# Performance work log

Hardware: AMD Instinct MI355X
Metric: run time of the kernel (lower is better)

## Reference

```python
import jax, jax.numpy as jnp
import numpy as np

N_GRAPHS = 256
EPS = 1e-5


def _bn(x, g, b):
    # training-mode BatchNorm1d: biased batch statistics
    m = jnp.mean(x, axis=0)
    v = jnp.mean((x - m) ** 2, axis=0)
    return (x - m) * jax.lax.rsqrt(v + EPS) * g + b


def _gcn_conv(x, W, b, src, dst, dinv, n_nodes):
    # GCNConv: D^{-1/2} (A + I) D^{-1/2} X W + b
    h = x @ W  # [N, H]
    coef = dinv[src] * dinv[dst]  # [E]
    msg = h[src] * coef[:, None]  # [E, H]
    agg = jax.ops.segment_sum(msg, dst, num_segments=n_nodes)
    agg = agg + h * (dinv * dinv)[:, None]  # self-loop term
    return agg + b


def setup_inputs() -> dict:
    key = jax.random.key(0)
    ks = jax.random.split(key, 20)
    N, E, D, H, C = 50000, 600000, 128, 128, 10
    L = 3  # num_conv_layers
    x = jax.random.normal(ks[0], (N, D), dtype=jnp.float32)
    edge_index = jax.random.randint(ks[1], (2, E), 0, N, dtype=jnp.int64)
    batch = jnp.sort(jax.random.randint(ks[2], (N,), 0, N_GRAPHS, dtype=jnp.int64))

    def xavier(k, shape):
        fan_in, fan_out = shape[0], shape[1]
        lim = float(np.sqrt(6.0 / (fan_in + fan_out)))
        return jax.random.uniform(k, shape, jnp.float32, -lim, lim)

    return {
        "x": x,
        "edge_index": edge_index,
        "batch": batch,
        "bn_feat_g": jnp.ones((D,), jnp.float32),
        "bn_feat_b": jnp.full((D,), 1e-4, jnp.float32),
        "conv_feat_W": xavier(ks[3], (D, H)),
        "conv_feat_b": jnp.zeros((H,), jnp.float32),
        "conv_W": jnp.stack([xavier(ks[4 + i], (H, H)) for i in range(L)]),
        "conv_b": jnp.zeros((L, H), jnp.float32),
        "bn_conv_g": jnp.ones((L, H), jnp.float32),
        "bn_conv_b": jnp.full((L, H), 1e-4, jnp.float32),
        "gate_W1": xavier(ks[8], (H, H)),
        "gate_b1": jnp.zeros((H,), jnp.float32),
        "gate_W2": xavier(ks[9], (H, 1)),
        "gate_b2": jnp.zeros((1,), jnp.float32),
        "fc_W": xavier(ks[10], (H, H)),
        "fc_b": jnp.zeros((H,), jnp.float32),
        "bn_fc_g": jnp.ones((H,), jnp.float32),
        "bn_fc_b": jnp.full((H,), 1e-4, jnp.float32),
        "cls_W": xavier(ks[11], (H, C)),
        "cls_b": jnp.zeros((C,), jnp.float32),
    }


def reference(x, edge_index, batch, bn_feat_g, bn_feat_b, conv_feat_W, conv_feat_b,
              conv_W, conv_b, bn_conv_g, bn_conv_b, gate_W1, gate_b1, gate_W2,
              gate_b2, fc_W, fc_b, bn_fc_g, bn_fc_b, cls_W, cls_b):
    N = x.shape[0]
    src, dst = edge_index[0], edge_index[1]
    # degree incl. self-loop (edge weights = 1)
    deg = jax.ops.segment_sum(jnp.ones_like(src, dtype=x.dtype), dst, num_segments=N) + 1.0
    dinv = jax.lax.rsqrt(deg)

    h = _bn(x, bn_feat_g, bn_feat_b)
    h = jax.nn.relu(_gcn_conv(h, conv_feat_W, conv_feat_b, src, dst, dinv, N))
    for i in range(conv_W.shape[0]):
        h = jax.nn.relu(_gcn_conv(_bn(h, bn_conv_g[i], bn_conv_b[i]),
                                  conv_W[i], conv_b[i], src, dst, dinv, N))
    gate = jax.nn.sigmoid(jax.nn.relu(h @ gate_W1 + gate_b1) @ gate_W2 + gate_b2)  # [N,1]
    g = jax.ops.segment_sum(h * gate, batch, num_segments=N_GRAPHS)  # [G, H]
    g = jax.nn.relu(_bn(g, bn_fc_g, bn_fc_b) @ fc_W + fc_b)
    logits = g @ cls_W + cls_b
    return jax.nn.log_softmax(logits, axis=-1)
```

## Files before the change

kernel.cpp:

```cpp
#include <hip/hip_runtime.h>
#include <hip/hip_fp16.h>

typedef unsigned short u16;
typedef unsigned int u32;
typedef __attribute__((ext_vector_type(8))) short short8;
typedef __attribute__((ext_vector_type(4))) float floatx4;

#define EPSI 1e-5f

__device__ __forceinline__ float b2f(u16 h) { return __uint_as_float(((u32)h) << 16); }
__device__ __forceinline__ u16 f2b(float f) {
    u32 u = __float_as_uint(f);
    return (u16)((u + 0x7fffu + ((u >> 16) & 1u)) >> 16);
}
__device__ __forceinline__ u32 pack2(float a, float b) {
    return (u32)f2b(a) | ((u32)f2b(b) << 16);
}
__device__ __forceinline__ float ldf(const void* p, int i, int fm) {
    if (fm == 1) return b2f(((const u16*)p)[i]);
    if (fm == 2) return __half2float(__ushort_as_half(((const u16*)p)[i]));
    return ((const float*)p)[i];
}
__device__ __forceinline__ int ldi(const void* p, int i, int im) {
    return im ? ((const int*)p)[2 * i] : ((const int*)p)[i];
}

__global__ void init_kernel(u32* zp, int nz, const void* ones, const void* ei, int* flags) {
    int i = blockIdx.x * 256 + threadIdx.x;
    if (i < nz) zp[i] = 0;
    if (blockIdx.x == 0 && threadIdx.x == 0) {
        u32 w = ((const u32*)ones)[0];
        int fm = 0;
        if (w == 0x3F803F80u) fm = 1;
        else if (w == 0x3C003C00u) fm = 2;
        const u32* e = (const u32*)ei;
        int all0 = 1;
        for (int k = 0; k < 16; ++k)
            if (e[2 * k + 1] != 0u) all0 = 0;
        flags[0] = fm;
        flags[1] = all0;
    }
}

__global__ void bigprep_kernel(const void* __restrict__ ei, int* __restrict__ cnt, int E,
                               const void* __restrict__ batch, int* __restrict__ bounds, int N,
                               int EB, const void* __restrict__ x, u32* __restrict__ A2,
                               float* __restrict__ stats0, const void* __restrict__ gW1,
                               const void* __restrict__ gb1, u16* __restrict__ Wtg,
                               float* __restrict__ bias2g, const void* __restrict__ cfW,
                               const void* __restrict__ cW, float* __restrict__ WTf,
                               const void* __restrict__ fcW, float* __restrict__ fcWf,
                               const void* __restrict__ clsW, float* __restrict__ clsWf,
                               const void* __restrict__ fcb, float* __restrict__ fcbf,
                               const void* __restrict__ clsb, float* __restrict__ clsbf,
                               const void* __restrict__ gW2, float* __restrict__ gW2f,
                               const void* __restrict__ gb2, float* __restrict__ gb2f,
                               const int* __restrict__ flags) {
    int fm = flags[0];
    int bid = blockIdx.x, t = threadIdx.x;
    if (bid < EB) {
        int im = flags[1];
        int g = bid * 256 + t;
        if (g < E) atomicAdd(&cnt[ldi(ei, E + g, im)], 1);
        if (g < N) {
            int b = ldi(batch, g, im);
            if (g == 0) {
                for (int q = 0; q <= b; ++q) bounds[q] = 0;
            } else {
                int bp = ldi(batch, g - 1, im);
                for (int q = bp + 1; q <= b; ++q) bounds[q] = g;
            }
            if (g == N - 1) {
                for (int q = b + 1; q <= 256; ++q) bounds[q] = N;
            }
        }
        return;
    }
    int pid = bid - EB;
    if (pid < 512) {
        int np = N * 64;
        float s0 = 0.f, s1 = 0.f, q0 = 0.f, q1 = 0.f;
        if (fm == 1) {
            const u32* xs = (const u32*)x;
            for (int j = pid * 256 + t; j < np; j += 512 * 256) {
                u32 w = xs[j];
                A2[j] = w;
                float v0 = b2f((u16)w), v1 = b2f((u16)(w >> 16));
                s0 += v0;
                q0 += v0 * v0;
                s1 += v1;
                q1 += v1 * v1;
            }
        } else {
            for (int j = pid * 256 + t; j < np; j += 512 * 256) {
                float v0 = ldf(x, 2 * j, fm);
                float v1 = ldf(x, 2 * j + 1, fm);
                A2[j] = pack2(v0, v1);
                s0 += v0;
                q0 += v0 * v0;
                s1 += v1;
                q1 += v1 * v1;
            }
        }
        __shared__ float2 sh[256];
        sh[t] = make_float2(s0, s1);
        __syncthreads();
        float* so = stats0 + (pid & 7) * 256;
        if (t < 64) {
            float a = 0.f, b = 0.f;
#pragma unroll
            for (int w = 0; w < 4; ++w) {
                float2 v = sh[t + w * 64];
                a += v.x;
                b += v.y;
            }
            atomicAdd(&so[2 * t], a);
            atomicAdd(&so[2 * t + 1], b);
        }
        __syncthreads();
        sh[t] = make_float2(q0, q1);
        __syncthreads();
        if (t < 64) {
            float a = 0.f, b = 0.f;
#pragma unroll
            for (int w = 0; w < 4; ++w) {
                float2 v = sh[t + w * 64];
                a += v.x;
                b += v.y;
            }
            atomicAdd(&so[128 + 2 * t], a);
            atomicAdd(&so[128 + 2 * t + 1], b);
        }
    } else if (pid < 640) {
        int n = pid - 512;
        if (t < 128) Wtg[n * 128 + t] = f2b(ldf(gW1, t * 128 + n, fm));
        if (t == 0) bias2g[n] = ldf(gb1, n, fm);
    } else if (pid < 704) {
        int task = pid - 640;
        int mat = task >> 4, tile = task & 15;
        int tr = (tile >> 2) * 32, tc = (tile & 3) * 32;
        const void* src = mat == 0 ? cfW : cW;
        int soff = mat == 0 ? 0 : (mat - 1) * 16384;
        __shared__ float tb[32][33];
#pragma unroll
        for (int i = 0; i < 4; ++i) {
            int o = t * 4 + i;
            int r = o >> 5, c = o & 31;
            tb[r][c] = ldf(src, soff + (tr + r) * 128 + tc + c, fm);
        }
        __syncthreads();
        float* dst = WTf + mat * 16384;
#pragma unroll
        for (int i = 0; i < 4; ++i) {
            int o = t * 4 + i;
            int nr = o >> 5, kc = o & 31;
            dst[(tc + nr) * 128 + tr + kc] = tb[kc][nr];
        }
    } else if (pid < 712) {
        int base = (pid - 704) * 2048;
        for (int i = t; i < 2048; i += 256) fcWf[base + i] = ldf(fcW, base + i, fm);
    } else {
        for (int i = t; i < 1280; i += 256) clsWf[i] = ldf(clsW, i, fm);
        if (t < 128) {
            fcbf[t] = ldf(fcb, t, fm);
            gW2f[t] = ldf(gW2, t, fm);
        }
        if (t < 10) clsbf[t] = ldf(clsb, t, fm);
        if (t == 0) gb2f[0] = ldf(gb2, 0, fm);
    }
}

__global__ void scan_part_kernel(const int* __restrict__ cnt, int* __restrict__ part, int n) {
    int b = blockIdx.x, t = threadIdx.x;
    int base = b * 1024 + t * 4;
    int s = 0;
#pragma unroll
    for (int j = 0; j < 4; ++j) {
        int idx = base + j;
        if (idx < n) s += cnt[idx];
    }
    __shared__ int sh[256];
    sh[t] = s;
    __syncthreads();
    for (int o = 128; o > 0; o >>= 1) {
        if (t < o) sh[t] += sh[t + o];
        __syncthreads();
    }
    if (t == 0) part[b] = sh[0];
}

__global__ void scan_local_wprep_kernel(const int* __restrict__ cnt,
                                        const int* __restrict__ part,
                                        int* __restrict__ row_start, int n, int NB,
                                        const float* __restrict__ stats0,
                                        const void* __restrict__ bng,
                                        const void* __restrict__ bnb,
                                        const float* __restrict__ WTf, u16* __restrict__ Wt,
                                        float* __restrict__ bias2, int N,
                                        const int* __restrict__ flags) {
    int b = blockIdx.x, t = threadIdx.x;
    __shared__ int sh[256];
    if (b == NB) {
        int fm = flags[0];
        __shared__ float scl[128], shl[128];
        if (t < 128) {
            float ms = 0.f, qs = 0.f;
#pragma unroll
            for (int c = 0; c < 8; ++c) {
                ms += stats0[c * 256 + t];
                qs += stats0[c * 256 + 128 + t];
            }
            float m = ms / (float)N;
            float var = qs / (float)N - m * m;
            float rs = rsqrtf(var + EPSI);
            float sc = rs * ldf(bng, t, fm);
            scl[t] = sc;
            shl[t] = ldf(bnb, t, fm) - m * sc;
        }
        __syncthreads();
        for (int idx = t; idx < 16384; idx += 256) Wt[idx] = f2b(scl[idx & 127] * WTf[idx]);
        if (t < 128) {
            float acc = 0.f;
#pragma unroll 8
            for (int k = 0; k < 128; ++k) acc += shl[k] * WTf[t * 128 + k];
            bias2[t] = acc;
        }
        return;
    }
    sh[t] = (t < b) ? part[t] : 0;
    __syncthreads();
    for (int o = 128; o > 0; o >>= 1) {
        if (t < o) sh[t] += sh[t + o];
        __syncthreads();
    }
    int pre = sh[0];
    __syncthreads();
    int base = b * 1024 + t * 4;
    int v[4];
    int s = 0;
#pragma unroll
    for (int j = 0; j < 4; ++j) {
        int idx = base + j;
        v[j] = (idx < n) ? cnt[idx] : 0;
        s += v[j];
    }
    sh[t] = s;
    __syncthreads();
    for (int o = 1; o < 256; o <<= 1) {
        int add = (t >= o) ? sh[t - o] : 0;
        __syncthreads();
        sh[t] += add;
        __syncthreads();
    }
    int run = pre + sh[t] - s;
#pragma unroll
    for (int j = 0; j < 4; ++j) {
        int idx = base + j;
        run += v[j];
        if (idx < n) row_start[idx + 1] = run;
    }
    if (b == 0 && t == 0) row_start[0] = 0;
}

__global__ void wprep_kernel(const float* __restrict__ stats, const void* __restrict__ bng,
                             const void* __restrict__ bnb, int poff,
                             const float* __restrict__ WTf, u16* __restrict__ Wt,
                             float* __restrict__ bias2, int N, const int* __restrict__ flags) {
    int fm = flags[0];
    int n = blockIdx.x, k = threadIdx.x;
    float ms = 0.f, qs = 0.f;
#pragma unroll
    for (int c = 0; c < 8; ++c) {
        ms += stats[c * 256 + k];
        qs += stats[c * 256 + 128 + k];
    }
    float m = ms / (float)N;
    float var = qs / (float)N - m * m;
    float rs = rsqrtf(var + EPSI);
    float sc = rs * ldf(bng, poff + k, fm);
    float sh = ldf(bnb, poff + k, fm) - m * sc;
    float w = WTf[n * 128 + k];
    Wt[n * 128 + k] = f2b(sc * w);
    __shared__ float red[128];
    red[k] = sh * w;
    __syncthreads();
    for (int o = 64; o > 0; o >>= 1) {
        if (k < o) red[k] += red[k + o];
        __syncthreads();
    }
    if (k == 0) bias2[n] = red[0];
}

__global__ __launch_bounds__(256) void mfma_fill_kernel(
    const u16* __restrict__ A, const u16* __restrict__ Wt, const float* __restrict__ bias2,
    u16* __restrict__ C, int N, int mmgrid, const void* __restrict__ ei,
    const int* __restrict__ row_start, int* __restrict__ fill_cnt, const int* __restrict__ cnt,
    int* __restrict__ col_idx, float* __restrict__ coef, int E,
    const int* __restrict__ flags) {
    int t = threadIdx.x;
    if ((int)blockIdx.x >= mmgrid) {
        int im = flags[1];
        int e = (blockIdx.x - mmgrid) * 256 + t;
        if (e < E) {
            int s = ldi(ei, e, im);
            int d = ldi(ei, E + e, im);
            int p = row_start[d] + atomicAdd(&fill_cnt[d], 1);
            col_idx[p] = s;
            coef[p] = rsqrtf((float)cnt[s] + 1.0f) * rsqrtf((float)cnt[d] + 1.0f);
        }
        return;
    }
    int wid = t >> 6, lane = t & 63;
    int m16 = lane & 15, q = lane >> 4;
    int row0 = blockIdx.x * 64 + wid * 16;
    if (row0 >= N) return;
    int arow = row0 + m16;
    floatx4 acc[8];
#pragma unroll
    for (int i = 0; i < 8; ++i) acc[i] = (floatx4){0.f, 0.f, 0.f, 0.f};
#pragma unroll
    for (int kc = 0; kc < 4; ++kc) {
        short8 af;
        if (arow < N) {
            af = *(const short8*)&A[(size_t)arow * 128 + kc * 32 + q * 8];
        } else {
#pragma unroll
            for (int j = 0; j < 8; ++j) af[j] = 0;
        }
#pragma unroll
        for (int nt = 0; nt < 8; ++nt) {
            short8 bf = *(const short8*)&Wt[(nt * 16 + m16) * 128 + kc * 32 + q * 8];
            acc[nt] = __builtin_amdgcn_mfma_f32_16x16x32_bf16(af, bf, acc[nt], 0, 0, 0);
        }
    }
#pragma unroll
    for (int nt = 0; nt < 8; ++nt) {
        float b2v = bias2[nt * 16 + m16];
#pragma unroll
        for (int reg = 0; reg < 4; ++reg) {
            int r = row0 + q * 4 + reg;
            if (r < N) C[(size_t)r * 128 + nt * 16 + m16] = f2b(acc[nt][reg] + b2v);
        }
    }
}

__global__ __launch_bounds__(256) void mfma_mm_kernel(
    const u16* __restrict__ A, const u16* __restrict__ Wt, const float* __restrict__ bias2,
    u16* __restrict__ C, float* __restrict__ gate, const float* __restrict__ gW2f,
    const float* __restrict__ gb2f, int N, int mode) {
    int t = threadIdx.x;
    int wid = t >> 6, lane = t & 63;
    int m16 = lane & 15, q = lane >> 4;
    int row0 = blockIdx.x * 64 + wid * 16;
    if (row0 >= N) return;
    int arow = row0 + m16;
    floatx4 acc[8];
#pragma unroll
    for (int i = 0; i < 8; ++i) acc[i] = (floatx4){0.f, 0.f, 0.f, 0.f};
#pragma unroll
    for (int kc = 0; kc < 4; ++kc) {
        short8 af;
        if (arow < N) {
            af = *(const short8*)&A[(size_t)arow * 128 + kc * 32 + q * 8];
        } else {
#pragma unroll
            for (int j = 0; j < 8; ++j) af[j] = 0;
        }
#pragma unroll
        for (int nt = 0; nt < 8; ++nt) {
            short8 bf = *(const short8*)&Wt[(nt * 16 + m16) * 128 + kc * 32 + q * 8];
            acc[nt] = __builtin_amdgcn_mfma_f32_16x16x32_bf16(af, bf, acc[nt], 0, 0, 0);
        }
    }
    if (mode == 0) {
#pragma unroll
        for (int nt = 0; nt < 8; ++nt) {
            float b2v = bias2[nt * 16 + m16];
#pragma unroll
            for (int reg = 0; reg < 4; ++reg) {
                int r = row0 + q * 4 + reg;
                if (r < N) C[(size_t)r * 128 + nt * 16 + m16] = f2b(acc[nt][reg] + b2v);
            }
        }
    } else {
        float p[4] = {0.f, 0.f, 0.f, 0.f};
#pragma unroll
        for (int nt = 0; nt < 8; ++nt) {
            float b2v = bias2[nt * 16 + m16];
            float w2v = gW2f[nt * 16 + m16];
#pragma unroll
            for (int reg = 0; reg < 4; ++reg)
                p[reg] += fmaxf(acc[nt][reg] + b2v, 0.0f) * w2v;
        }
        float gb = gb2f[0];
#pragma unroll
        for (int reg = 0; reg < 4; ++reg) {
            float v = p[reg];
            v += __shfl_xor(v, 1);
            v += __shfl_xor(v, 2);
            v += __shfl_xor(v, 4);
            v += __shfl_xor(v, 8);
            if (m16 == 0) {
                int r = row0 + q * 4 + reg;
                if (r < N) gate[r] = 1.0f / (1.0f + expf(-(v + gb)));
            }
        }
    }
}

__global__ __launch_bounds__(1024) void agg_kernel(
    const u32* __restrict__ C2, const int* __restrict__ row_start,
    const int* __restrict__ col_idx, const float* __restrict__ coef,
    const int* __restrict__ cnt, const void* __restrict__ bias, int boff,
    u32* __restrict__ A2, float* __restrict__ statsOut, int N,
    const int* __restrict__ flags) {
    int fm = flags[0];
    int t = threadIdx.x;
    int wid = t >> 6, lane = t & 63;
    int node = blockIdx.x * 16 + wid;
    float ax = 0.f, ay = 0.f;
    if (node < N) {
        float d2 = 1.0f / ((float)cnt[node] + 1.0f);
        u32 selfw = C2[(size_t)node * 64 + lane];
        ax = b2f((u16)selfw) * d2;
        ay = b2f((u16)(selfw >> 16)) * d2;
        int rs = row_start[node], re = row_start[node + 1];
        int e = rs;
        for (; e + 8 <= re; e += 8) {
            int si[8];
            float wi[8];
            u32 vi[8];
#pragma unroll
            for (int j = 0; j < 8; ++j) {
                si[j] = col_idx[e + j];
                wi[j] = coef[e + j];
            }
#pragma unroll
            for (int j = 0; j < 8; ++j) vi[j] = C2[(size_t)si[j] * 64 + lane];
#pragma unroll
            for (int j = 0; j < 8; ++j) {
                ax += b2f((u16)vi[j]) * wi[j];
                ay += b2f((u16)(vi[j] >> 16)) * wi[j];
            }
        }
        for (; e + 4 <= re; e += 4) {
            int s0 = col_idx[e + 0], s1 = col_idx[e + 1];
            int s2 = col_idx[e + 2], s3 = col_idx[e + 3];
            float w0 = coef[e + 0], w1 = coef[e + 1];
            float w2 = coef[e + 2], w3 = coef[e + 3];
            u32 v0 = C2[(size_t)s0 * 64 + lane];
            u32 v1 = C2[(size_t)s1 * 64 + lane];
            u32 v2 = C2[(size_t)s2 * 64 + lane];
            u32 v3 = C2[(size_t)s3 * 64 + lane];
            ax += b2f((u16)v0) * w0 + b2f((u16)v1) * w1 + b2f((u16)v2) * w2 + b2f((u16)v3) * w3;
            ay += b2f((u16)(v0 >> 16)) * w0 + b2f((u16)(v1 >> 16)) * w1 +
                  b2f((u16)(v2 >> 16)) * w2 + b2f((u16)(v3 >> 16)) * w3;
        }
        for (; e < re; ++e) {
            int s = col_idx[e];
            float w = coef[e];
            u32 v = C2[(size_t)s * 64 + lane];
            ax += b2f((u16)v) * w;
            ay += b2f((u16)(v >> 16)) * w;
        }
        int f = lane * 2;
        ax = fmaxf(ax + ldf(bias, boff + f, fm), 0.0f);
        ay = fmaxf(ay + ldf(bias, boff + f + 1, fm), 0.0f);
        A2[(size_t)node * 64 + lane] = pack2(ax, ay);
    }
    __shared__ float2 sh[1024];
    sh[t] = make_float2(ax, ay);
    __syncthreads();
    float* so = statsOut + (blockIdx.x & 7) * 256;
    if (t < 64) {
        float a = 0.f, b = 0.f;
#pragma unroll
        for (int w = 0; w < 16; ++w) {
            float2 v = sh[t + w * 64];
            a += v.x;
            b += v.y;
        }
        atomicAdd(&so[2 * t], a);
        atomicAdd(&so[2 * t + 1], b);
    }
    __syncthreads();
    sh[t] = make_float2(ax * ax, ay * ay);
    __syncthreads();
    if (t < 64) {
        float a = 0.f, b = 0.f;
#pragma unroll
        for (int w = 0; w < 16; ++w) {
            float2 v = sh[t + w * 64];
            a += v.x;
            b += v.y;
        }
        atomicAdd(&so[128 + 2 * t], a);
        atomicAdd(&so[128 + 2 * t + 1], b);
    }
}

__global__ void pool_kernel(const u16* __restrict__ A, const float* __restrict__ gate,
                            const int* __restrict__ bounds, float* __restrict__ pooled,
                            float* __restrict__ statsP) {
    int g = blockIdx.x;
    int t = threadIdx.x;
    int f = t & 127, half = t >> 7;
    int s = bounds[g], e = bounds[g + 1];
    float acc = 0.f;
    for (int r = s + half; r < e; r += 2) acc += b2f(A[(size_t)r * 128 + f]) * gate[r];
    __shared__ float sh[256];
    sh[t] = acc;
    __syncthreads();
    if (t < 128) {
        float v = sh[t] + sh[t + 128];
        pooled[g * 128 + t] = v;
        float* so = statsP + (g & 7) * 256;
        atomicAdd(&so[t], v);
        atomicAdd(&so[128 + t], v * v);
    }
}

__global__ __launch_bounds__(256) void fc_cls_kernel(
    const float* __restrict__ pooled, const float* __restrict__ statsP,
    const void* __restrict__ bng, const void* __restrict__ bnb,
    const float* __restrict__ fcWf, const float* __restrict__ fcbf,
    const float* __restrict__ clsWf, const float* __restrict__ clsbf, void* __restrict__ out,
    const int* __restrict__ flags) {
    int fm = flags[0];
    int g = blockIdx.x, t = threadIdx.x;
    __shared__ float pv[128];
    __shared__ float red[256];
    __shared__ float fco[128];
    __shared__ float lg[10];
    __shared__ float redv[2];
    if (t < 128) {
        float ms = 0.f, qs = 0.f;
#pragma unroll
        for (int c = 0; c < 8; ++c) {
            ms += statsP[c * 256 + t];
            qs += statsP[c * 256 + 128 + t];
        }
        float m = ms / 256.0f;
        float var = qs / 256.0f - m * m;
        float rs = rsqrtf(var + EPSI);
        float sc = rs * ldf(bng, t, fm);
        pv[t] = pooled[g * 128 + t] * sc + (ldf(bnb, t, fm) - m * sc);
    }
    __syncthreads();
    {
        int j = t & 127, half = t >> 7;
        float acc = 0.f;
        int k0 = half * 64;
#pragma unroll 8
        for (int k = k0; k < k0 + 64; ++k) acc += pv[k] * fcWf[k * 128 + j];
        red[t] = acc;
    }
    __syncthreads();
    if (t < 128) fco[t] = fmaxf(red[t] + red[t + 128] + fcbf[t], 0.0f);
    __syncthreads();
    if (t < 10) {
        float a = clsbf[t];
#pragma unroll 8
        for (int k = 0; k < 128; ++k) a += fco[k] * clsWf[k * 10 + t];
        lg[t] = a;
    }
    __syncthreads();
    if (t == 0) {
        float mx = lg[0];
        for (int j = 1; j < 10; ++j) mx = fmaxf(mx, lg[j]);
        float se = 0.f;
        for (int j = 0; j < 10; ++j) se += expf(lg[j] - mx);
        redv[0] = mx;
        redv[1] = logf(se);
    }
    __syncthreads();
    if (t < 10) {
        float v = lg[t] - redv[0] - redv[1];
        if (fm == 1) ((u16*)out)[g * 10 + t] = f2b(v);
        else if (fm == 2) ((u16*)out)[g * 10 + t] = __half_as_ushort(__float2half(v));
        else ((float*)out)[g * 10 + t] = v;
    }
}

extern "C" void kernel_launch(void* const* d_in, const int* in_sizes, int n_in,
                              void* d_out, int out_size, void* d_ws, size_t ws_size,
                              hipStream_t stream) {
    const void* x = d_in[0];
    const void* ei = d_in[1];
    const void* batch = d_in[2];
    const void* bn_feat_g = d_in[3];
    const void* bn_feat_b = d_in[4];
    const void* conv_feat_W = d_in[5];
    const void* conv_feat_b = d_in[6];
    const void* conv_W = d_in[7];
    const void* conv_b = d_in[8];
    const void* bn_conv_g = d_in[9];
    const void* bn_conv_b = d_in[10];
    const void* gate_W1 = d_in[11];
    const void* gate_b1 = d_in[12];
    const void* gate_W2 = d_in[13];
    const void* gate_b2 = d_in[14];
    const void* fc_W = d_in[15];
    const void* fc_b = d_in[16];
    const void* bn_fc_g = d_in[17];
    const void* bn_fc_b = d_in[18];
    const void* cls_W = d_in[19];
    const void* cls_b = d_in[20];

    const int N = in_sizes[2];
    const int E = in_sizes[1] / 2;
    const int NB = (N + 1023) / 1024;
    const int EB = ((E > N ? E : N) + 255) / 256;

    u32* ws = (u32*)d_ws;
    size_t off = 0;
    auto alloc = [&](size_t n) {
        size_t o = off;
        off += (n + 63) & ~(size_t)63;
        return o;
    };
    size_t o_cnt = alloc(N);
    size_t o_fill = alloc(N);
    size_t o_stats = alloc(5 * 2048);
    size_t o_statsP = alloc(2048);
    size_t zero_end = off;
    size_t o_flags = alloc(16);
    size_t o_part = alloc(256);
    size_t o_rs = alloc((size_t)N + 1);
    size_t o_col = alloc(E);
    size_t o_coef = alloc(E);
    size_t o_wt = alloc(128 * 128 / 2);
    size_t o_b2 = alloc(128);
    size_t o_wtg = alloc(128 * 128 / 2);
    size_t o_b2g = alloc(128);
    size_t o_WTf = alloc(4 * 16384);
    size_t o_fcW = alloc(16384);
    size_t o_fcb = alloc(128);
    size_t o_clsW = alloc(1280);
    size_t o_clsb = alloc(16);
    size_t o_gW2 = alloc(128);
    size_t o_gb2 = alloc(16);
    size_t o_gate = alloc(N);
    size_t o_bnd = alloc(257);
    size_t o_pool = alloc(256 * 128);
    size_t o_A = alloc((size_t)N * 64);
    size_t o_C = alloc((size_t)N * 64);
    (void)ws_size;
    (void)n_in;
    (void)out_size;

    int* cnt = (int*)(ws + o_cnt);
    int* fillc = (int*)(ws + o_fill);
    float* stats = (float*)(ws + o_stats);
    float* statsP = (float*)(ws + o_statsP);
    int* flags = (int*)(ws + o_flags);
    int* part = (int*)(ws + o_part);
    int* row_start = (int*)(ws + o_rs);
    int* col_idx = (int*)(ws + o_col);
    float* coef = (float*)(ws + o_coef);
    u16* Wt = (u16*)(ws + o_wt);
    float* bias2 = (float*)(ws + o_b2);
    u16* Wtg = (u16*)(ws + o_wtg);
    float* bias2g = (float*)(ws + o_b2g);
    float* WTf = (float*)(ws + o_WTf);
    float* fcWf = (float*)(ws + o_fcW);
    float* fcbf = (float*)(ws + o_fcb);
    float* clsWf = (float*)(ws + o_clsW);
    float* clsbf = (float*)(ws + o_clsb);
    float* gW2f = (float*)(ws + o_gW2);
    float* gb2f = (float*)(ws + o_gb2);
    float* gateb = (float*)(ws + o_gate);
    int* bnd = (int*)(ws + o_bnd);
    float* pooled = (float*)(ws + o_pool);
    u16* A = (u16*)(ws + o_A);
    u16* C = (u16*)(ws + o_C);

    int nz = (int)zero_end;
    init_kernel<<<(nz + 255) / 256, 256, 0, stream>>>(ws, nz, bn_feat_g, ei, flags);
    bigprep_kernel<<<EB + 713, 256, 0, stream>>>(
        ei, cnt, E, batch, bnd, N, EB, x, (u32*)A, stats, gate_W1, gate_b1, Wtg, bias2g,
        conv_feat_W, conv_W, WTf, fc_W, fcWf, cls_W, clsWf, fc_b, fcbf, cls_b, clsbf, gate_W2,
        gW2f, gate_b2, gb2f, flags);
    scan_part_kernel<<<NB, 256, 0, stream>>>(cnt, part, N);
    scan_local_wprep_kernel<<<NB + 1, 256, 0, stream>>>(cnt, part, row_start, N, NB, stats,
                                                        bn_feat_g, bn_feat_b, WTf, Wt, bias2, N,
                                                        flags);

    int mmgrid = (N + 63) / 64;
    int agggrid = (N + 15) / 16;
    mfma_fill_kernel<<<mmgrid + EB, 256, 0, stream>>>(A, Wt, bias2, C, N, mmgrid, ei, row_start,
                                                      fillc, cnt, col_idx, coef, E, flags);
    for (int l = 0; l < 4; ++l) {
        const void* bb = l ? conv_b : conv_feat_b;
        int poff = l ? (l - 1) * 128 : 0;
        if (l > 0) {
            wprep_kernel<<<128, 128, 0, stream>>>(stats + (size_t)l * 2048, bn_conv_g,
                                                  bn_conv_b, (l - 1) * 128,
                                                  WTf + (size_t)l * 16384, Wt, bias2, N, flags);
            mfma_mm_kernel<<<mmgrid, 256, 0, stream>>>(A, Wt, bias2, C, nullptr, nullptr,
                                                       nullptr, N, 0);
        }
        agg_kernel<<<agggrid, 1024, 0, stream>>>((const u32*)C, row_start, col_idx, coef, cnt,
                                                 bb, poff, (u32*)A,
                                                 stats + (size_t)(l + 1) * 2048, N, flags);
    }

    mfma_mm_kernel<<<mmgrid, 256, 0, stream>>>(A, Wtg, bias2g, nullptr, gateb, gW2f, gb2f, N, 2);
    pool_kernel<<<256, 256, 0, stream>>>(A, gateb, bnd, pooled, statsP);
    fc_cls_kernel<<<256, 256, 0, stream>>>(pooled, statsP, bn_fc_g, bn_fc_b, fcWf, fcbf, clsWf,
                                           clsbf, d_out, flags);
}
```

Before: 518.0 us.

## Fuse BN weight prep into GEMMs, merge scan, pack CSR edges

Removes the separate wprep kernels by having each MFMA GEMM compute the BatchNorm scale/shift from the stats itself and apply it to A on load, with weights pre-transposed to bf16 once. The two-pass scan becomes a single kernel that sums the preceding counts directly. Column indices and coefficients are packed into int2 edges so aggregation does one load per edge, and the final agg skips unused stats reduction. This cuts several launches at the cost of extra per-element ALU and redundant prefix reads in the scan, and it changes rounding because normalization now happens in bf16 before the MFMA.

Result: faster. 491.1 us (-5.2%).

```diff
diff --git a/kernel.cpp b/kernel.cpp
--- a/kernel.cpp
+++ b/kernel.cpp
@@ -48,7 +48,7 @@
                                float* __restrict__ stats0, const void* __restrict__ gW1,
                                const void* __restrict__ gb1, u16* __restrict__ Wtg,
                                float* __restrict__ bias2g, const void* __restrict__ cfW,
-                               const void* __restrict__ cW, float* __restrict__ WTf,
+                               const void* __restrict__ cW, u16* __restrict__ Wt4,
                                const void* __restrict__ fcW, float* __restrict__ fcWf,
                                const void* __restrict__ clsW, float* __restrict__ clsWf,
                                const void* __restrict__ fcb, float* __restrict__ fcbf,
@@ -149,12 +149,12 @@
             tb[r][c] = ldf(src, soff + (tr + r) * 128 + tc + c, fm);
         }
         __syncthreads();
-        float* dst = WTf + mat * 16384;
+        u16* dst = Wt4 + mat * 16384;
 #pragma unroll
         for (int i = 0; i < 4; ++i) {
             int o = t * 4 + i;
             int nr = o >> 5, kc = o & 31;
-            dst[(tc + nr) * 128 + tr + kc] = tb[kc][nr];
+            dst[(tc + nr) * 128 + tr + kc] = f2b(tb[kc][nr]);
         }
     } else if (pid < 712) {
         int base = (pid - 704) * 2048;
@@ -170,64 +170,17 @@
     }
 }
 
-__global__ void scan_part_kernel(const int* __restrict__ cnt, int* __restrict__ part, int n) {
-    int b = blockIdx.x, t = threadIdx.x;
-    int base = b * 1024 + t * 4;
-    int s = 0;
-#pragma unroll
-    for (int j = 0; j < 4; ++j) {
-        int idx = base + j;
-        if (idx < n) s += cnt[idx];
-    }
-    __shared__ int sh[256];
-    sh[t] = s;
-    __syncthreads();
-    for (int o = 128; o > 0; o >>= 1) {
-        if (t < o) sh[t] += sh[t + o];
-        __syncthreads();
-    }
-    if (t == 0) part[b] = sh[0];
-}
-
-__global__ void scan_local_wprep_kernel(const int* __restrict__ cnt,
-                                        const int* __restrict__ part,
-                                        int* __restrict__ row_start, int n, int NB,
-                                        const float* __restrict__ stats0,
-                                        const void* __restrict__ bng,
-                                        const void* __restrict__ bnb,
-                                        const float* __restrict__ WTf, u16* __restrict__ Wt,
-                                        float* __restrict__ bias2, int N,
-                                        const int* __restrict__ flags) {
+__global__ void scan_kernel(const int* __restrict__ cnt, int* __restrict__ row_start, int n) {
     int b = blockIdx.x, t = threadIdx.x;
     __shared__ int sh[256];
-    if (b == NB) {
-        int fm = flags[0];
-        __shared__ float scl[128], shl[128];
-        if (t < 128) {
-            float ms = 0.f, qs = 0.f;
-#pragma unroll
-            for (int c = 0; c < 8; ++c) {
-                ms += stats0[c * 256 + t];
-                qs += stats0[c * 256 + 128 + t];
-            }
-            float m = ms / (float)N;
-            float var = qs / (float)N - m * m;
-            float rs = rsqrtf(var + EPSI);
-            float sc = rs * ldf(bng, t, fm);
-            scl[t] = sc;
-            shl[t] = ldf(bnb, t, fm) - m * sc;
-        }
-        __syncthreads();
-        for (int idx = t; idx < 16384; idx += 256) Wt[idx] = f2b(scl[idx & 127] * WTf[idx]);
-        if (t < 128) {
-            float acc = 0.f;
-#pragma unroll 8
-            for (int k = 0; k < 128; ++k) acc += shl[k] * WTf[t * 128 + k];
-            bias2[t] = acc;
-        }
-        return;
-    }
-    sh[t] = (t < b) ? part[t] : 0;
+    const int4* c4 = (const int4*)cnt;
+    int lim4 = b * 256;
+    int acc = 0;
+    for (int i = t; i < lim4; i += 256) {
+        int4 v = c4[i];
+        acc += v.x + v.y + v.z + v.w;
+    }
+    sh[t] = acc;
     __syncthreads();
     for (int o = 128; o > 0; o >>= 1) {
         if (t < o) sh[t] += sh[t + o];
@@ -262,40 +215,11 @@
     if (b == 0 && t == 0) row_start[0] = 0;
 }
 
-__global__ void wprep_kernel(const float* __restrict__ stats, const void* __restrict__ bng,
-                             const void* __restrict__ bnb, int poff,
-                             const float* __restrict__ WTf, u16* __restrict__ Wt,
-                             float* __restrict__ bias2, int N, const int* __restrict__ flags) {
-    int fm = flags[0];
-    int n = blockIdx.x, k = threadIdx.x;
-    float ms = 0.f, qs = 0.f;
-#pragma unroll
-    for (int c = 0; c < 8; ++c) {
-        ms += stats[c * 256 + k];
-        qs += stats[c * 256 + 128 + k];
-    }
-    float m = ms / (float)N;
-    float var = qs / (float)N - m * m;
-    float rs = rsqrtf(var + EPSI);
-    float sc = rs * ldf(bng, poff + k, fm);
-    float sh = ldf(bnb, poff + k, fm) - m * sc;
-    float w = WTf[n * 128 + k];
-    Wt[n * 128 + k] = f2b(sc * w);
-    __shared__ float red[128];
-    red[k] = sh * w;
-    __syncthreads();
-    for (int o = 64; o > 0; o >>= 1) {
-        if (k < o) red[k] += red[k + o];
-        __syncthreads();
-    }
-    if (k == 0) bias2[n] = red[0];
-}
-
 __global__ __launch_bounds__(256) void mfma_fill_kernel(
-    const u16* __restrict__ A, const u16* __restrict__ Wt, const float* __restrict__ bias2,
-    u16* __restrict__ C, int N, int mmgrid, const void* __restrict__ ei,
-    const int* __restrict__ row_start, int* __restrict__ fill_cnt, const int* __restrict__ cnt,
-    int* __restrict__ col_idx, float* __restrict__ coef, int E,
+    const u16* __restrict__ A, const u16* __restrict__ Wt, const float* __restrict__ stats,
+    const void* __restrict__ bng, const void* __restrict__ bnb, u16* __restrict__ C, int N,
+    int mmgrid, const void* __restrict__ ei, const int* __restrict__ row_start,
+    int* __restrict__ fill_cnt, const int* __restrict__ cnt, int2* __restrict__ edges, int E,
     const int* __restrict__ flags) {
     int t = threadIdx.x;
     if ((int)blockIdx.x >= mmgrid) {
@@ -305,11 +229,28 @@
             int s = ldi(ei, e, im);
             int d = ldi(ei, E + e, im);
             int p = row_start[d] + atomicAdd(&fill_cnt[d], 1);
-            col_idx[p] = s;
-            coef[p] = rsqrtf((float)cnt[s] + 1.0f) * rsqrtf((float)cnt[d] + 1.0f);
+            float cf = rsqrtf((float)cnt[s] + 1.0f) * rsqrtf((float)cnt[d] + 1.0f);
+            edges[p] = make_int2(s, __float_as_int(cf));
         }
         return;
     }
+    int fm = flags[0];
+    __shared__ float scs[128], shs[128];
+    if (t < 128) {
+        float ms = 0.f, qs = 0.f;
+#pragma unroll
+        for (int c = 0; c < 8; ++c) {
+            ms += stats[c * 256 + t];
+            qs += stats[c * 256 + 128 + t];
+        }
+        float m = ms / (float)N;
+        float var = qs / (float)N - m * m;
+        float rs = rsqrtf(var + EPSI);
+        float sc = rs * ldf(bng, t, fm);
+        scs[t] = sc;
+        shs[t] = ldf(bnb, t, fm) - m * sc;
+    }
+    __syncthreads();
     int wid = t >> 6, lane = t & 63;
     int m16 = lane & 15, q = lane >> 4;
     int row0 = blockIdx.x * 64 + wid * 16;
@@ -322,7 +263,11 @@
     for (int kc = 0; kc < 4; ++kc) {
         short8 af;
         if (arow < N) {
-            af = *(const short8*)&A[(size_t)arow * 128 + kc * 32 + q * 8];
+            short8 raw = *(const short8*)&A[(size_t)arow * 128 + kc * 32 + q * 8];
+            int k0 = kc * 32 + q * 8;
+#pragma unroll
+            for (int j = 0; j < 8; ++j)
+                af[j] = (short)f2b(b2f((u16)raw[j]) * scs[k0 + j] + shs[k0 + j]);
         } else {
 #pragma unroll
             for (int j = 0; j < 8; ++j) af[j] = 0;
@@ -335,20 +280,38 @@
     }
 #pragma unroll
     for (int nt = 0; nt < 8; ++nt) {
-        float b2v = bias2[nt * 16 + m16];
 #pragma unroll
         for (int reg = 0; reg < 4; ++reg) {
             int r = row0 + q * 4 + reg;
-            if (r < N) C[(size_t)r * 128 + nt * 16 + m16] = f2b(acc[nt][reg] + b2v);
+            if (r < N) C[(size_t)r * 128 + nt * 16 + m16] = f2b(acc[nt][reg]);
         }
     }
 }
 
 __global__ __launch_bounds__(256) void mfma_mm_kernel(
-    const u16* __restrict__ A, const u16* __restrict__ Wt, const float* __restrict__ bias2,
-    u16* __restrict__ C, float* __restrict__ gate, const float* __restrict__ gW2f,
-    const float* __restrict__ gb2f, int N, int mode) {
+    const u16* __restrict__ A, const u16* __restrict__ Wt, const float* __restrict__ stats,
+    const void* __restrict__ bng, const void* __restrict__ bnb, int poff,
+    const float* __restrict__ bias2, u16* __restrict__ C, float* __restrict__ gate,
+    const float* __restrict__ gW2f, const float* __restrict__ gb2f, int N, int mode,
+    const int* __restrict__ flags) {
     int t = threadIdx.x;
+    __shared__ float scs[128], shs[128];
+    if (stats && t < 128) {
+        int fm = flags[0];
+        float ms = 0.f, qs = 0.f;
+#pragma unroll
+        for (int c = 0; c < 8; ++c) {
+            ms += stats[c * 256 + t];
+            qs += stats[c * 256 + 128 + t];
+        }
+        float m = ms / (float)N;
+        float var = qs / (float)N - m * m;
+        float rs = rsqrtf(var + EPSI);
+        float sc = rs * ldf(bng, poff + t, fm);
+        scs[t] = sc;
+        shs[t] = ldf(bnb, poff + t, fm) - m * sc;
+    }
+    __syncthreads();
     int wid = t >> 6, lane = t & 63;
     int m16 = lane & 15, q = lane >> 4;
     int row0 = blockIdx.x * 64 + wid * 16;
@@ -361,7 +324,15 @@
     for (int kc = 0; kc < 4; ++kc) {
         short8 af;
         if (arow < N) {
-            af = *(const short8*)&A[(size_t)arow * 128 + kc * 32 + q * 8];
+            if (stats) {
+                short8 raw = *(const short8*)&A[(size_t)arow * 128 + kc * 32 + q * 8];
+                int k0 = kc * 32 + q * 8;
+#pragma unroll
+                for (int j = 0; j < 8; ++j)
+                    af[j] = (short)f2b(b2f((u16)raw[j]) * scs[k0 + j] + shs[k0 + j]);
+            } else {
+                af = *(const short8*)&A[(size_t)arow * 128 + kc * 32 + q * 8];
+            }
         } else {
 #pragma unroll
             for (int j = 0; j < 8; ++j) af[j] = 0;
@@ -375,11 +346,10 @@
     if (mode == 0) {
 #pragma unroll
         for (int nt = 0; nt < 8; ++nt) {
-            float b2v = bias2[nt * 16 + m16];
 #pragma unroll
             for (int reg = 0; reg < 4; ++reg) {
                 int r = row0 + q * 4 + reg;
-                if (r < N) C[(size_t)r * 128 + nt * 16 + m16] = f2b(acc[nt][reg] + b2v);
+                if (r < N) C[(size_t)r * 128 + nt * 16 + m16] = f2b(acc[nt][reg]);
             }
         }
     } else {
@@ -410,10 +380,9 @@
 
 __global__ __launch_bounds__(1024) void agg_kernel(
     const u32* __restrict__ C2, const int* __restrict__ row_start,
-    const int* __restrict__ col_idx, const float* __restrict__ coef,
-    const int* __restrict__ cnt, const void* __restrict__ bias, int boff,
-    u32* __restrict__ A2, float* __restrict__ statsOut, int N,
-    const int* __restrict__ flags) {
+    const int2* __restrict__ edges, const int* __restrict__ cnt,
+    const void* __restrict__ bias, int boff, u32* __restrict__ A2,
+    float* __restrict__ statsOut, int N, const int* __restrict__ flags) {
     int fm = flags[0];
     int t = threadIdx.x;
     int wid = t >> 6, lane = t & 63;
@@ -427,39 +396,35 @@
         int rs = row_start[node], re = row_start[node + 1];
         int e = rs;
         for (; e + 8 <= re; e += 8) {
-            int si[8];
-            float wi[8];
+            int2 ed[8];
             u32 vi[8];
 #pragma unroll
+            for (int j = 0; j < 8; ++j) ed[j] = edges[e + j];
+#pragma unroll
+            for (int j = 0; j < 8; ++j) vi[j] = C2[(size_t)ed[j].x * 64 + lane];
+#pragma unroll
             for (int j = 0; j < 8; ++j) {
-                si[j] = col_idx[e + j];
-                wi[j] = coef[e + j];
-            }
-#pragma unroll
-            for (int j = 0; j < 8; ++j) vi[j] = C2[(size_t)si[j] * 64 + lane];
-#pragma unroll
-            for (int j = 0; j < 8; ++j) {
-                ax += b2f((u16)vi[j]) * wi[j];
-                ay += b2f((u16)(vi[j] >> 16)) * wi[j];
+                float w = __int_as_float(ed[j].y);
+                ax += b2f((u16)vi[j]) * w;
+                ay += b2f((u16)(vi[j] >> 16)) * w;
             }
         }
         for (; e + 4 <= re; e += 4) {
-            int s0 = col_idx[e + 0], s1 = col_idx[e + 1];
-            int s2 = col_idx[e + 2], s3 = col_idx[e + 3];
-            float w0 = coef[e + 0], w1 = coef[e + 1];
-            float w2 = coef[e + 2], w3 = coef[e + 3];
-            u32 v0 = C2[(size_t)s0 * 64 + lane];
-            u32 v1 = C2[(size_t)s1 * 64 + lane];
-            u32 v2 = C2[(size_t)s2 * 64 + lane];
-            u32 v3 = C2[(size_t)s3 * 64 + lane];
+            int2 e0 = edges[e + 0], e1 = edges[e + 1], e2 = edges[e + 2], e3 = edges[e + 3];
+            u32 v0 = C2[(size_t)e0.x * 64 + lane];
+            u32 v1 = C2[(size_t)e1.x * 64 + lane];
+            u32 v2 = C2[(size_t)e2.x * 64 + lane];
+            u32 v3 = C2[(size_t)e3.x * 64 + lane];
+            float w0 = __int_as_float(e0.y), w1 = __int_as_float(e1.y);
+            float w2 = __int_as_float(e2.y), w3 = __int_as_float(e3.y);
             ax += b2f((u16)v0) * w0 + b2f((u16)v1) * w1 + b2f((u16)v2) * w2 + b2f((u16)v3) * w3;
             ay += b2f((u16)(v0 >> 16)) * w0 + b2f((u16)(v1 >> 16)) * w1 +
                   b2f((u16)(v2 >> 16)) * w2 + b2f((u16)(v3 >> 16)) * w3;
         }
         for (; e < re; ++e) {
-            int s = col_idx[e];
-            float w = coef[e];
-            u32 v = C2[(size_t)s * 64 + lane];
+            int2 ed = edges[e];
+            float w = __int_as_float(ed.y);
+            u32 v = C2[(size_t)ed.x * 64 + lane];
             ax += b2f((u16)v) * w;
             ay += b2f((u16)(v >> 16)) * w;
         }
@@ -468,6 +433,7 @@
         ay = fmaxf(ay + ldf(bias, boff + f + 1, fm), 0.0f);
         A2[(size_t)node * 64 + lane] = pack2(ax, ay);
     }
+    if (!statsOut) return;
     __shared__ float2 sh[1024];
     sh[t] = make_float2(ax, ay);
     __syncthreads();
@@ -625,15 +591,11 @@
     size_t o_statsP = alloc(2048);
     size_t zero_end = off;
     size_t o_flags = alloc(16);
-    size_t o_part = alloc(256);
     size_t o_rs = alloc((size_t)N + 1);
-    size_t o_col = alloc(E);
-    size_t o_coef = alloc(E);
-    size_t o_wt = alloc(128 * 128 / 2);
-    size_t o_b2 = alloc(128);
+    size_t o_edges = alloc((size_t)E * 2);
     size_t o_wtg = alloc(128 * 128 / 2);
     size_t o_b2g = alloc(128);
-    size_t o_WTf = alloc(4 * 16384);
+    size_t o_Wt4 = alloc(4 * 16384 / 2);
     size_t o_fcW = alloc(16384);
     size_t o_fcb = alloc(128);
     size_t o_clsW = alloc(1280);
@@ -654,15 +616,11 @@
     float* stats = (float*)(ws + o_stats);
     float* statsP = (float*)(ws + o_statsP);
     int* flags = (int*)(ws + o_flags);
-    int* part = (int*)(ws + o_part);
     int* row_start = (int*)(ws + o_rs);
-    int* col_idx = (int*)(ws + o_col);
-    float* coef = (float*)(ws + o_coef);
-    u16* Wt = (u16*)(ws + o_wt);
-    float* bias2 = (float*)(ws + o_b2);
+    int2* edges = (int2*)(ws + o_edges);
     u16* Wtg = (u16*)(ws + o_wtg);
     float* bias2g = (float*)(ws + o_b2g);
-    float* WTf = (float*)(ws + o_WTf);
+    u16* Wt4 = (u16*)(ws + o_Wt4);
     float* fcWf = (float*)(ws + o_fcW);
     float* fcbf = (float*)(ws + o_fcb);
     float* clsWf = (float*)(ws + o_clsW);
@@ -679,33 +637,29 @@
     init_kernel<<<(nz + 255) / 256, 256, 0, stream>>>(ws, nz, bn_feat_g, ei, flags);
     bigprep_kernel<<<EB + 713, 256, 0, stream>>>(
         ei, cnt, E, batch, bnd, N, EB, x, (u32*)A, stats, gate_W1, gate_b1, Wtg, bias2g,
-        conv_feat_W, conv_W, WTf, fc_W, fcWf, cls_W, clsWf, fc_b, fcbf, cls_b, clsbf, gate_W2,
+        conv_feat_W, conv_W, Wt4, fc_W, fcWf, cls_W, clsWf, fc_b, fcbf, cls_b, clsbf, gate_W2,
         gW2f, gate_b2, gb2f, flags);
-    scan_part_kernel<<<NB, 256, 0, stream>>>(cnt, part, N);
-    scan_local_wprep_kernel<<<NB + 1, 256, 0, stream>>>(cnt, part, row_start, N, NB, stats,
-                                                        bn_feat_g, bn_feat_b, WTf, Wt, bias2, N,
-                                                        flags);
+    scan_kernel<<<NB, 256, 0, stream>>>(cnt, row_start, N);
 
     int mmgrid = (N + 63) / 64;
     int agggrid = (N + 15) / 16;
-    mfma_fill_kernel<<<mmgrid + EB, 256, 0, stream>>>(A, Wt, bias2, C, N, mmgrid, ei, row_start,
-                                                      fillc, cnt, col_idx, coef, E, flags);
+    mfma_fill_kernel<<<mmgrid + EB, 256, 0, stream>>>(A, Wt4, stats, bn_feat_g, bn_feat_b, C, N,
+                                                      mmgrid, ei, row_start, fillc, cnt, edges,
+                                                      E, flags);
     for (int l = 0; l < 4; ++l) {
         const void* bb = l ? conv_b : conv_feat_b;
         int poff = l ? (l - 1) * 128 : 0;
-        if (l > 0) {
-            wprep_kernel<<<128, 128, 0, stream>>>(stats + (size_t)l * 2048, bn_conv_g,
-                                                  bn_conv_b, (l - 1) * 128,
-                                                  WTf + (size_t)l * 16384, Wt, bias2, N, flags);
-            mfma_mm_kernel<<<mmgrid, 256, 0, stream>>>(A, Wt, bias2, C, nullptr, nullptr,
-                                                       nullptr, N, 0);
-        }
-        agg_kernel<<<agggrid, 1024, 0, stream>>>((const u32*)C, row_start, col_idx, coef, cnt,
-                                                 bb, poff, (u32*)A,
-                                                 stats + (size_t)(l + 1) * 2048, N, flags);
-    }
-
-    mfma_mm_kernel<<<mmgrid, 256, 0, stream>>>(A, Wtg, bias2g, nullptr, gateb, gW2f, gb2f, N, 2);
+        if (l > 0)
+            mfma_mm_kernel<<<mmgrid, 256, 0, stream>>>(
+                A, Wt4 + (size_t)l * 16384, stats + (size_t)l * 2048, bn_conv_g, bn_conv_b,
+                (l - 1) * 128, nullptr, C, nullptr, nullptr, nullptr, N, 0, flags);
+        float* so = (l < 3) ? stats + (size_t)(l + 1) * 2048 : nullptr;
+        agg_kernel<<<agggrid, 1024, 0, stream>>>((const u32*)C, row_start, edges, cnt, bb, poff,
+                                                 (u32*)A, so, N, flags);
+    }
+
+    mfma_mm_kernel<<<mmgrid, 256, 0, stream>>>(A, Wtg, nullptr, nullptr, nullptr, 0, bias2g,
+                                               nullptr, gateb, gW2f, gb2f, N, 2, flags);
     pool_kernel<<<256, 256, 0, stream>>>(A, gateb, bnd, pooled, statsP);
     fc_cls_kernel<<<256, 256, 0, stream>>>(pooled, statsP, bn_fc_g, bn_fc_b, fcWf, fcbf, clsWf,
                                            clsbf, d_out, flags);
```
